# Kernel optimization log

Hardware: AMD Instinct MI355X
Metric: run time of the kernel (lower is better)

## Reference

```python
import jax, jax.numpy as jnp
import numpy as np

EPS = 1e-5

def layer_norm(x, g, b):
    m = jnp.mean(x, axis=-1, keepdims=True)
    v = jnp.var(x, axis=-1, keepdims=True)
    return (x - m) * jax.lax.rsqrt(v + EPS) * g + b

def setup_inputs() -> dict:
    key = jax.random.key(0)
    ks = jax.random.split(key, 10)
    A, T, c_s, c_z, c_atom, c_pair = 1024, 256, 384, 128, 128, 16
    tok = jax.random.randint(ks[0], (A,), 0, T)
    a2t = jax.nn.one_hot(tok, T, dtype=jnp.float32)  # [A, T] one-hot atom->token map
    return {
        "atom_to_token_index": a2t,
        "cl": jax.random.normal(ks[1], (A, c_atom), jnp.float32),
        "plm": jax.random.normal(ks[2], (A, A, c_pair), jnp.float32),
        "ql": jax.random.normal(ks[3], (A, c_atom), jnp.float32),
        "s_trunk": jax.random.normal(ks[4], (T, c_s), jnp.float32),
        "zij": jax.random.normal(ks[5], (T, T, c_z), jnp.float32),
        "rl": jax.random.normal(ks[6], (A, 3), jnp.float32),
        "ln_s_g": jnp.ones((c_s,), jnp.float32),
        "ln_s_b": jnp.zeros((c_s,), jnp.float32),
        "W_s": jax.random.normal(ks[7], (c_s, c_atom), jnp.float32) / np.sqrt(c_s),
        "ln_z_g": jnp.ones((c_z,), jnp.float32),
        "ln_z_b": jnp.zeros((c_z,), jnp.float32),
        "W_z": jax.random.normal(ks[8], (c_z, c_pair), jnp.float32) / np.sqrt(c_z),
        "W_r": jax.random.normal(ks[9], (3, c_atom), jnp.float32) / np.sqrt(3.0),
    }

def reference(atom_to_token_index, cl, plm, ql, s_trunk, zij, rl,
              ln_s_g, ln_s_b, W_s, ln_z_g, ln_z_b, W_z, W_r):
    a2t = atom_to_token_index  # [A, T]
    # token -> atom gather of single rep: sum_t a2t[a,t] * s_trunk[t,:]  -> [A, c_s]
    s_atom = jnp.einsum('at,tc->ac', a2t, s_trunk)
    cl = cl + layer_norm(s_atom, ln_s_g, ln_s_b) @ W_s  # [A, c_atom]
    # token-pair -> atom-pair gather: sum_{t,u} a2t[a,t] a2t[b,u] zij[t,u,:]
    # factored into two one-hot contractions (same math as the dense one-hot outer product)
    z_half = jnp.einsum('at,tuz->auz', a2t, zij)      # [A, T, c_z]
    z_atom = jnp.einsum('auz,bu->abz', z_half, a2t)    # [A, A, c_z]
    plm = plm + layer_norm(z_atom, ln_z_g, ln_z_b) @ W_z  # [A, A, c_pair]
    ql = ql + rl @ W_r  # [A, c_atom]
    return (cl, plm, ql)
```

## Files before the change

kernel.cpp:

```cpp
#include <hip/hip_runtime.h>

#define A_N 1024
#define T_N 256
#define CS 384
#define CZ 128
#define CA 128
#define CP 16
#define LN_EPS 1e-5f

typedef __bf16  bf16x8 __attribute__((ext_vector_type(8)));
typedef float   f32x4  __attribute__((ext_vector_type(4)));

__global__ __launch_bounds__(128) void s_kernel(
        const float* __restrict__ s_trunk,
        const float* __restrict__ g,
        const float* __restrict__ b,
        const float* __restrict__ W_s,
        float* __restrict__ Ys) {
    int t = blockIdx.x, tid = threadIdx.x;
    __shared__ float xs[CS];
    __shared__ float2 wred[2];
    float sum = 0.f, sq = 0.f;
    #pragma unroll
    for (int j = 0; j < 3; ++j) {
        float v = s_trunk[t * CS + j * 128 + tid];
        xs[j * 128 + tid] = v;
        sum += v; sq += v * v;
    }
    #pragma unroll
    for (int off = 32; off > 0; off >>= 1) {
        sum += __shfl_down(sum, off);
        sq  += __shfl_down(sq,  off);
    }
    if ((tid & 63) == 0) wred[tid >> 6] = make_float2(sum, sq);
    __syncthreads();
    float s  = wred[0].x + wred[1].x;
    float ss = wred[0].y + wred[1].y;
    float m = s * (1.f / CS);
    float rstd = rsqrtf(ss * (1.f / CS) - m * m + LN_EPS);

    float a0 = 0.f, a1 = 0.f, a2 = 0.f, a3 = 0.f;
    for (int k = 0; k < CS; k += 4) {
        float z0 = (xs[k + 0] - m) * rstd * g[k + 0] + b[k + 0];
        float z1 = (xs[k + 1] - m) * rstd * g[k + 1] + b[k + 1];
        float z2 = (xs[k + 2] - m) * rstd * g[k + 2] + b[k + 2];
        float z3 = (xs[k + 3] - m) * rstd * g[k + 3] + b[k + 3];
        a0 = fmaf(z0, W_s[(k + 0) * CA + tid], a0);
        a1 = fmaf(z1, W_s[(k + 1) * CA + tid], a1);
        a2 = fmaf(z2, W_s[(k + 2) * CA + tid], a2);
        a3 = fmaf(z3, W_s[(k + 3) * CA + tid], a3);
    }
    Ys[t * CA + tid] = (a0 + a1) + (a2 + a3);
}

#define WSTRIDE 136

__global__ __launch_bounds__(256) void z_mfma_kernel(
        const float* __restrict__ zij,
        const float* __restrict__ g,
        const float* __restrict__ b,
        const float* __restrict__ W_z,
        float* __restrict__ Yz) {
    __shared__ __bf16 wb[CP * WSTRIDE];
    __shared__ float2 gb_part[16][16];
    __shared__ float Gw_sh[CP], Bw_sh[CP];

    int t = threadIdx.x;

    {
        int j = t & 15, seg = t >> 4;
        float sg = 0.f, sb = 0.f;
        #pragma unroll
        for (int i = 0; i < 8; ++i) {
            int k = seg * 8 + i;
            float w = W_z[k * CP + j];
            float gw = g[k] * w;
            wb[j * WSTRIDE + k] = (__bf16)gw;
            sg += gw;
            sb = fmaf(b[k], w, sb);
        }
        gb_part[seg][j] = make_float2(sg, sb);
    }
    __syncthreads();
    if (t < CP) {
        float sg = 0.f, sb = 0.f;
        #pragma unroll
        for (int s = 0; s < 16; ++s) { float2 p = gb_part[s][t]; sg += p.x; sb += p.y; }
        Gw_sh[t] = sg; Bw_sh[t] = sb;
    }

    int wave = t >> 6, lane = t & 63;
    int m    = lane & 15, quad = lane >> 4;
    size_t grow = (size_t)blockIdx.x * 64 + wave * 16 + m;

    const float4* zrow = (const float4*)(zij + grow * CZ);
    float4 xv[8];
    #pragma unroll
    for (int s = 0; s < 4; ++s) {
        xv[2 * s]     = zrow[quad * 2 + 8 * s];
        xv[2 * s + 1] = zrow[quad * 2 + 8 * s + 1];
    }

    float sum = 0.f, sq = 0.f;
    #pragma unroll
    for (int i = 0; i < 8; ++i) {
        float4 v = xv[i];
        sum += (v.x + v.y) + (v.z + v.w);
        sq  += v.x * v.x + v.y * v.y + v.z * v.z + v.w * v.w;
    }
    sum += __shfl_xor(sum, 16);  sq += __shfl_xor(sq, 16);
    sum += __shfl_xor(sum, 32);  sq += __shfl_xor(sq, 32);
    float mval = sum * (1.f / CZ);
    float rstd = rsqrtf(sq * (1.f / CZ) - mval * mval + LN_EPS);

    __syncthreads();

    f32x4 acc = {0.f, 0.f, 0.f, 0.f};
    #pragma unroll
    for (int s = 0; s < 4; ++s) {
        float4 v0 = xv[2 * s], v1 = xv[2 * s + 1];
        bf16x8 af;
        af[0] = (__bf16)v0.x; af[1] = (__bf16)v0.y;
        af[2] = (__bf16)v0.z; af[3] = (__bf16)v0.w;
        af[4] = (__bf16)v1.x; af[5] = (__bf16)v1.y;
        af[6] = (__bf16)v1.z; af[7] = (__bf16)v1.w;
        bf16x8 bf = *(const bf16x8*)&wb[m * WSTRIDE + quad * 8 + 32 * s];
        acc = __builtin_amdgcn_mfma_f32_16x16x32_bf16(af, bf, acc, 0, 0, 0);
    }

    float gwj = Gw_sh[m], bwj = Bw_sh[m];
    size_t obase = (size_t)blockIdx.x * 64 + wave * 16;
    #pragma unroll
    for (int i = 0; i < 4; ++i) {
        int r = quad * 4 + i;
        float mi = __shfl(mval, r);
        float ri = __shfl(rstd, r);
        float y = ri * (acc[i] - mi * gwj) + bwj;
        Yz[(obase + r) * CP + m] = y;
    }
}

__global__ __launch_bounds__(128) void atom_kernel(
        const float* __restrict__ a2t,
        const float* __restrict__ cl,
        const float* __restrict__ ql,
        const float* __restrict__ rl,
        const float* __restrict__ Ys,
        const float* __restrict__ W_r,
        int* __restrict__ tok,
        float* __restrict__ out_cl,
        float* __restrict__ out_ql) {
    int a = blockIdx.x, tid = threadIdx.x;
    __shared__ int ta_sh;
    float v0 = a2t[a * T_N + tid];
    float v1 = a2t[a * T_N + 128 + tid];
    if (v0 > 0.5f) ta_sh = tid;
    if (v1 > 0.5f) ta_sh = 128 + tid;
    __syncthreads();
    int ta = ta_sh;
    if (tid == 0) tok[a] = ta;

    out_cl[a * CA + tid] = cl[a * CA + tid] + Ys[ta * CA + tid];

    float r0 = rl[a * 3 + 0], r1 = rl[a * 3 + 1], r2 = rl[a * 3 + 2];
    out_ql[a * CA + tid] = ql[a * CA + tid]
                         + r0 * W_r[tid] + r1 * W_r[CA + tid] + r2 * W_r[2 * CA + tid];
}

__global__ __launch_bounds__(256) void plm_kernel(
        const float* __restrict__ plm,
        const float* __restrict__ Yz,
        const int* __restrict__ tok,
        float* __restrict__ out) {
    int tid = threadIdx.x;
    size_t i = (size_t)blockIdx.x * 256 + tid;
    int ta = tok[blockIdx.x >> 4];
    int bb = ((blockIdx.x & 15) << 6) + (tid >> 2);
    int tb = tok[bb];
    float4 pv = ((const float4*)plm)[i];
    float4 yv = ((const float4*)(Yz + (size_t)(ta * T_N + tb) * CP))[tid & 3];
    float4 o;
    o.x = pv.x + yv.x; o.y = pv.y + yv.y;
    o.z = pv.z + yv.z; o.w = pv.w + yv.w;
    ((float4*)out)[i] = o;
}

extern "C" void kernel_launch(void* const* d_in, const int* in_sizes, int n_in,
                              void* d_out, int out_size, void* d_ws, size_t ws_size,
                              hipStream_t stream) {
    const float* a2t     = (const float*)d_in[0];
    const float* cl      = (const float*)d_in[1];
    const float* plm     = (const float*)d_in[2];
    const float* ql      = (const float*)d_in[3];
    const float* s_trunk = (const float*)d_in[4];
    const float* zij     = (const float*)d_in[5];
    const float* rl      = (const float*)d_in[6];
    const float* ln_s_g  = (const float*)d_in[7];
    const float* ln_s_b  = (const float*)d_in[8];
    const float* W_s     = (const float*)d_in[9];
    const float* ln_z_g  = (const float*)d_in[10];
    const float* ln_z_b  = (const float*)d_in[11];
    const float* W_z     = (const float*)d_in[12];
    const float* W_r     = (const float*)d_in[13];

    int*   tok = (int*)d_ws;
    float* Ys  = (float*)((char*)d_ws + 4096);
    float* Yz  = (float*)((char*)d_ws + 4096 + 131072);

    float* out_cl  = (float*)d_out;
    float* out_plm = out_cl + A_N * CA;
    float* out_ql  = out_plm + (size_t)A_N * A_N * CP;

    s_kernel<<<T_N, 128, 0, stream>>>(s_trunk, ln_s_g, ln_s_b, W_s, Ys);
    z_mfma_kernel<<<(T_N * T_N) / 64, 256, 0, stream>>>(zij, ln_z_g, ln_z_b, W_z, Yz);
    atom_kernel<<<A_N, 128, 0, stream>>>(a2t, cl, ql, rl, Ys, W_r, tok, out_cl, out_ql);
    plm_kernel<<<((size_t)A_N * A_N * CP / 4) / 256, 256, 0, stream>>>(plm, Yz, tok, out_plm);
}
```

Before: 191.0 us.

## Merge four launches into two kernels and stage Yz row in shared memory

Folds the s-trunk projection, z-pair LayerNorm/MFMA projection and token-index extraction into one launch, with blocks split by blockIdx. The atom outputs and the plm broadcast-add move into a second kernel with one block per atom row. That block caches the token map and its Yz row in swizzled shared memory, replacing scattered global gathers. This removes two launches and the per-element global lookups of tok and Yz, at the cost of a 512-thread block with about 20KB of shared memory, which may limit occupancy.

```diff
diff --git a/kernel.cpp b/kernel.cpp
--- a/kernel.cpp
+++ b/kernel.cpp
@@ -11,87 +11,101 @@
 typedef __bf16  bf16x8 __attribute__((ext_vector_type(8)));
 typedef float   f32x4  __attribute__((ext_vector_type(4)));
 
-__global__ __launch_bounds__(128) void s_kernel(
+#define WSTRIDE 136
+
+__global__ __launch_bounds__(256) void token_kernel(
         const float* __restrict__ s_trunk,
-        const float* __restrict__ g,
-        const float* __restrict__ b,
+        const float* __restrict__ gs,
+        const float* __restrict__ bs,
         const float* __restrict__ W_s,
-        float* __restrict__ Ys) {
-    int t = blockIdx.x, tid = threadIdx.x;
+        float* __restrict__ Ys,
+        const float* __restrict__ zij,
+        const float* __restrict__ gz,
+        const float* __restrict__ bz,
+        const float* __restrict__ W_z,
+        float* __restrict__ Yz,
+        const float* __restrict__ a2t,
+        int* __restrict__ tok) {
     __shared__ float xs[CS];
-    __shared__ float2 wred[2];
-    float sum = 0.f, sq = 0.f;
-    #pragma unroll
-    for (int j = 0; j < 3; ++j) {
-        float v = s_trunk[t * CS + j * 128 + tid];
-        xs[j * 128 + tid] = v;
-        sum += v; sq += v * v;
-    }
-    #pragma unroll
-    for (int off = 32; off > 0; off >>= 1) {
-        sum += __shfl_down(sum, off);
-        sq  += __shfl_down(sq,  off);
-    }
-    if ((tid & 63) == 0) wred[tid >> 6] = make_float2(sum, sq);
-    __syncthreads();
-    float s  = wred[0].x + wred[1].x;
-    float ss = wred[0].y + wred[1].y;
-    float m = s * (1.f / CS);
-    float rstd = rsqrtf(ss * (1.f / CS) - m * m + LN_EPS);
-
-    float a0 = 0.f, a1 = 0.f, a2 = 0.f, a3 = 0.f;
-    for (int k = 0; k < CS; k += 4) {
-        float z0 = (xs[k + 0] - m) * rstd * g[k + 0] + b[k + 0];
-        float z1 = (xs[k + 1] - m) * rstd * g[k + 1] + b[k + 1];
-        float z2 = (xs[k + 2] - m) * rstd * g[k + 2] + b[k + 2];
-        float z3 = (xs[k + 3] - m) * rstd * g[k + 3] + b[k + 3];
-        a0 = fmaf(z0, W_s[(k + 0) * CA + tid], a0);
-        a1 = fmaf(z1, W_s[(k + 1) * CA + tid], a1);
-        a2 = fmaf(z2, W_s[(k + 2) * CA + tid], a2);
-        a3 = fmaf(z3, W_s[(k + 3) * CA + tid], a3);
-    }
-    Ys[t * CA + tid] = (a0 + a1) + (a2 + a3);
-}
-
-#define WSTRIDE 136
-
-__global__ __launch_bounds__(256) void z_mfma_kernel(
-        const float* __restrict__ zij,
-        const float* __restrict__ g,
-        const float* __restrict__ b,
-        const float* __restrict__ W_z,
-        float* __restrict__ Yz) {
+    __shared__ float2 sred[4];
+    __shared__ float part[2][128];
     __shared__ __bf16 wb[CP * WSTRIDE];
     __shared__ float2 gb_part[16][16];
     __shared__ float Gw_sh[CP], Bw_sh[CP];
 
-    int t = threadIdx.x;
+    int tid = threadIdx.x;
+
+    if (blockIdx.x < 256) {
+        int t = blockIdx.x;
+        float sum = 0.f, sq = 0.f;
+        {
+            float v = s_trunk[t * CS + tid];
+            xs[tid] = v; sum = v; sq = v * v;
+            if (tid < CS - 256) {
+                float v2 = s_trunk[t * CS + 256 + tid];
+                xs[256 + tid] = v2; sum += v2; sq += v2 * v2;
+            }
+        }
+        #pragma unroll
+        for (int off = 32; off > 0; off >>= 1) {
+            sum += __shfl_down(sum, off);
+            sq  += __shfl_down(sq,  off);
+        }
+        if ((tid & 63) == 0) sred[tid >> 6] = make_float2(sum, sq);
+        __syncthreads();
+        float s_ = sred[0].x + sred[1].x + sred[2].x + sred[3].x;
+        float ss = sred[0].y + sred[1].y + sred[2].y + sred[3].y;
+        float m = s_ * (1.f / CS);
+        float rstd = rsqrtf(ss * (1.f / CS) - m * m + LN_EPS);
+
+        int col = tid & 127, seg = tid >> 7;
+        float a0 = 0.f, a1 = 0.f, a2 = 0.f, a3 = 0.f;
+        int k0 = seg * (CS / 2);
+        for (int k = k0; k < k0 + CS / 2; k += 4) {
+            float z0 = (xs[k + 0] - m) * rstd * gs[k + 0] + bs[k + 0];
+            float z1 = (xs[k + 1] - m) * rstd * gs[k + 1] + bs[k + 1];
+            float z2 = (xs[k + 2] - m) * rstd * gs[k + 2] + bs[k + 2];
+            float z3 = (xs[k + 3] - m) * rstd * gs[k + 3] + bs[k + 3];
+            a0 = fmaf(z0, W_s[(k + 0) * CA + col], a0);
+            a1 = fmaf(z1, W_s[(k + 1) * CA + col], a1);
+            a2 = fmaf(z2, W_s[(k + 2) * CA + col], a2);
+            a3 = fmaf(z3, W_s[(k + 3) * CA + col], a3);
+        }
+        part[seg][col] = (a0 + a1) + (a2 + a3);
+        __syncthreads();
+        if (tid < 128) Ys[t * CA + tid] = part[0][tid] + part[1][tid];
+        return;
+    }
+
+    int a = blockIdx.x - 256;
+
+    { float v = a2t[(size_t)a * T_N + tid]; if (v > 0.5f) tok[a] = tid; }
 
     {
-        int j = t & 15, seg = t >> 4;
+        int j = tid & 15, seg = tid >> 4;
         float sg = 0.f, sb = 0.f;
         #pragma unroll
         for (int i = 0; i < 8; ++i) {
             int k = seg * 8 + i;
             float w = W_z[k * CP + j];
-            float gw = g[k] * w;
+            float gw = gz[k] * w;
             wb[j * WSTRIDE + k] = (__bf16)gw;
             sg += gw;
-            sb = fmaf(b[k], w, sb);
+            sb = fmaf(bz[k], w, sb);
         }
         gb_part[seg][j] = make_float2(sg, sb);
     }
     __syncthreads();
-    if (t < CP) {
+    if (tid < CP) {
         float sg = 0.f, sb = 0.f;
         #pragma unroll
-        for (int s = 0; s < 16; ++s) { float2 p = gb_part[s][t]; sg += p.x; sb += p.y; }
-        Gw_sh[t] = sg; Bw_sh[t] = sb;
-    }
-
-    int wave = t >> 6, lane = t & 63;
+        for (int s = 0; s < 16; ++s) { float2 p = gb_part[s][tid]; sg += p.x; sb += p.y; }
+        Gw_sh[tid] = sg; Bw_sh[tid] = sb;
+    }
+
+    int wave = tid >> 6, lane = tid & 63;
     int m    = lane & 15, quad = lane >> 4;
-    size_t grow = (size_t)blockIdx.x * 64 + wave * 16 + m;
+    size_t grow = (size_t)a * 64 + wave * 16 + m;
 
     const float4* zrow = (const float4*)(zij + grow * CZ);
     float4 xv[8];
@@ -124,12 +138,12 @@
         af[2] = (__bf16)v0.z; af[3] = (__bf16)v0.w;
         af[4] = (__bf16)v1.x; af[5] = (__bf16)v1.y;
         af[6] = (__bf16)v1.z; af[7] = (__bf16)v1.w;
-        bf16x8 bf = *(const bf16x8*)&wb[m * WSTRIDE + quad * 8 + 32 * s];
-        acc = __builtin_amdgcn_mfma_f32_16x16x32_bf16(af, bf, acc, 0, 0, 0);
+        bf16x8 bfv = *(const bf16x8*)&wb[m * WSTRIDE + quad * 8 + 32 * s];
+        acc = __builtin_amdgcn_mfma_f32_16x16x32_bf16(af, bfv, acc, 0, 0, 0);
     }
 
     float gwj = Gw_sh[m], bwj = Bw_sh[m];
-    size_t obase = (size_t)blockIdx.x * 64 + wave * 16;
+    size_t obase = (size_t)a * 64 + wave * 16;
     #pragma unroll
     for (int i = 0; i < 4; ++i) {
         int r = quad * 4 + i;
@@ -140,49 +154,59 @@
     }
 }
 
-__global__ __launch_bounds__(128) void atom_kernel(
-        const float* __restrict__ a2t,
+__global__ __launch_bounds__(512) void atom_plm_kernel(
+        const float* __restrict__ plm,
+        const float* __restrict__ Yz,
+        const int* __restrict__ tok,
         const float* __restrict__ cl,
         const float* __restrict__ ql,
         const float* __restrict__ rl,
         const float* __restrict__ Ys,
         const float* __restrict__ W_r,
-        int* __restrict__ tok,
         float* __restrict__ out_cl,
+        float* __restrict__ out_plm,
         float* __restrict__ out_ql) {
-    int a = blockIdx.x, tid = threadIdx.x;
-    __shared__ int ta_sh;
-    float v0 = a2t[a * T_N + tid];
-    float v1 = a2t[a * T_N + 128 + tid];
-    if (v0 > 0.5f) ta_sh = tid;
-    if (v1 > 0.5f) ta_sh = 128 + tid;
+    __shared__ int    tok_sh[A_N];
+    __shared__ float4 yz_sh[T_N * CP / 4];
+
+    int a = blockIdx.x;
+    int tid = threadIdx.x;
+    int ta = tok[a];
+
+    if (tid < 256) ((int4*)tok_sh)[tid] = ((const int4*)tok)[tid];
+
+    const float4* yrow = (const float4*)(Yz + (size_t)ta * (T_N * CP));
+    #pragma unroll
+    for (int p = 0; p < 2; ++p) {
+        int j = p * 512 + tid;
+        yz_sh[j ^ ((j >> 3) & 7)] = yrow[j];
+    }
+
+    if (tid < 128) {
+        out_cl[a * CA + tid] = cl[a * CA + tid] + Ys[ta * CA + tid];
+    } else if (tid < 256) {
+        int c = tid - 128;
+        float r0 = rl[a * 3 + 0], r1 = rl[a * 3 + 1], r2 = rl[a * 3 + 2];
+        out_ql[a * CA + c] = ql[a * CA + c]
+            + fmaf(r0, W_r[c], fmaf(r1, W_r[CA + c], r2 * W_r[2 * CA + c]));
+    }
     __syncthreads();
-    int ta = ta_sh;
-    if (tid == 0) tok[a] = ta;
-
-    out_cl[a * CA + tid] = cl[a * CA + tid] + Ys[ta * CA + tid];
-
-    float r0 = rl[a * 3 + 0], r1 = rl[a * 3 + 1], r2 = rl[a * 3 + 2];
-    out_ql[a * CA + tid] = ql[a * CA + tid]
-                         + r0 * W_r[tid] + r1 * W_r[CA + tid] + r2 * W_r[2 * CA + tid];
-}
-
-__global__ __launch_bounds__(256) void plm_kernel(
-        const float* __restrict__ plm,
-        const float* __restrict__ Yz,
-        const int* __restrict__ tok,
-        float* __restrict__ out) {
-    int tid = threadIdx.x;
-    size_t i = (size_t)blockIdx.x * 256 + tid;
-    int ta = tok[blockIdx.x >> 4];
-    int bb = ((blockIdx.x & 15) << 6) + (tid >> 2);
-    int tb = tok[bb];
-    float4 pv = ((const float4*)plm)[i];
-    float4 yv = ((const float4*)(Yz + (size_t)(ta * T_N + tb) * CP))[tid & 3];
-    float4 o;
-    o.x = pv.x + yv.x; o.y = pv.y + yv.y;
-    o.z = pv.z + yv.z; o.w = pv.w + yv.w;
-    ((float4*)out)[i] = o;
+
+    const float4* prow = (const float4*)(plm     + (size_t)a * (A_N * CP));
+    float4*       orow = (float4*)      (out_plm + (size_t)a * (A_N * CP));
+    #pragma unroll
+    for (int it = 0; it < 8; ++it) {
+        int f4 = it * 512 + tid;
+        int b  = f4 >> 2;
+        int tb = tok_sh[b];
+        int x  = tb * 4 + (f4 & 3);
+        float4 yv = yz_sh[x ^ ((x >> 3) & 7)];
+        float4 pv = prow[f4];
+        float4 o;
+        o.x = pv.x + yv.x; o.y = pv.y + yv.y;
+        o.z = pv.z + yv.z; o.w = pv.w + yv.w;
+        orow[f4] = o;
+    }
 }
 
 extern "C" void kernel_launch(void* const* d_in, const int* in_sizes, int n_in,
@@ -211,8 +235,11 @@
     float* out_plm = out_cl + A_N * CA;
     float* out_ql  = out_plm + (size_t)A_N * A_N * CP;
 
-    s_kernel<<<T_N, 128, 0, stream>>>(s_trunk, ln_s_g, ln_s_b, W_s, Ys);
-    z_mfma_kernel<<<(T_N * T_N) / 64, 256, 0, stream>>>(zij, ln_z_g, ln_z_b, W_z, Yz);
-    atom_kernel<<<A_N, 128, 0, stream>>>(a2t, cl, ql, rl, Ys, W_r, tok, out_cl, out_ql);
-    plm_kernel<<<((size_t)A_N * A_N * CP / 4) / 256, 256, 0, stream>>>(plm, Yz, tok, out_plm);
+    token_kernel<<<256 + A_N, 256, 0, stream>>>(
+        s_trunk, ln_s_g, ln_s_b, W_s, Ys,
+        zij, ln_z_g, ln_z_b, W_z, Yz,
+        a2t, tok);
+    atom_plm_kernel<<<A_N, 512, 0, stream>>>(
+        plm, Yz, tok, cl, ql, rl, Ys, W_r,
+        out_cl, out_plm, out_ql);
 }
```

New measurement: 182.4 us. -4.5%, faster.
